# Optimization experiments

Measured on AMD Instinct MI355X. Metric: run time of the kernel, lower is better.

## Reference

```python
import jax, jax.numpy as jnp
import numpy as np
from math import sqrt

B, T, C = 2, 2048, 2048
H = 16
NOPE, ROPE, VD, LORA = 128, 64, 128, 512
QK = NOPE + ROPE  # 192
EPS = 1e-6


def _make_freq_cis(T, rope_dim):
    inv = 1.0 / (10000.0 ** (np.arange(0, rope_dim, 2, dtype=np.float32) / rope_dim))
    t = np.arange(T, dtype=np.float32)
    ang = np.outer(t, inv)  # [T, rope_dim/2]
    return jnp.asarray(np.stack([np.cos(ang), np.sin(ang)], -1))  # [T, rope_dim/2, 2]


def setup_inputs() -> dict:
    key = jax.random.key(0)
    ks = jax.random.split(key, 6)
    x = jax.random.normal(ks[0], (B, T, C), jnp.float32)
    freq_cis = _make_freq_cis(T, ROPE)
    causal = jnp.where(jnp.tril(jnp.ones((T, T), bool)), 0.0, -1e9).astype(jnp.float32)
    Wq = jax.random.normal(ks[1], (C, H * QK), jnp.float32) * (1.0 / sqrt(C))
    Wckv = jax.random.normal(ks[2], (C, LORA + ROPE), jnp.float32) * (1.0 / sqrt(C))
    kv_norm_w = jnp.ones((LORA,), jnp.float32)
    Wdkv = jax.random.normal(ks[3], (LORA, H * (NOPE + VD)), jnp.float32) * (1.0 / sqrt(LORA))
    Wproj = jax.random.normal(ks[4], (H * VD, C), jnp.float32) * (1.0 / sqrt(H * VD))
    return {"x": x, "freq_cis": freq_cis, "mask": causal, "window": causal,
            "Wq": Wq, "Wckv": Wckv, "kv_norm_w": kv_norm_w, "Wdkv": Wdkv,
            "Wproj": Wproj, "start_pos": 0}


def apply_rope(x, freq_cis):
    # x: [B, T, h, D]; freq_cis: [T, D/2, 2]
    b, t, h, d = x.shape
    xr = x.reshape(b, t, h, d // 2, 2)
    fc = freq_cis.reshape(1, t, 1, d // 2, 2)
    real = xr[..., 0] * fc[..., 0] - xr[..., 1] * fc[..., 1]
    imag = xr[..., 1] * fc[..., 0] + xr[..., 0] * fc[..., 1]
    return jnp.stack([real, imag], -1).reshape(b, t, h, d)


def rms_norm(x, w, eps=EPS):
    return x * jax.lax.rsqrt(jnp.mean(x * x, -1, keepdims=True) + eps) * w


def reference(x, freq_cis, mask, window, Wq, Wckv, kv_norm_w, Wdkv, Wproj, start_pos):
    del window, start_pos  # Global attention, no KV cache (prefill)
    b, t, _ = x.shape
    q = (x @ Wq).reshape(b, t, H, QK)
    q_nope, q_rope = q[..., :NOPE], q[..., NOPE:]
    q_rope = apply_rope(q_rope, freq_cis)

    ckv = x @ Wckv  # [B, T, LORA+ROPE]
    kv_lat, k_rope = ckv[..., :LORA], ckv[..., LORA:]
    k_rope = apply_rope(k_rope.reshape(b, t, 1, ROPE), freq_cis)  # [B,T,1,ROPE]

    kv = rms_norm(kv_lat, kv_norm_w) @ Wdkv  # [B, T, H*(NOPE+VD)]
    kv = kv.reshape(b, t, H, NOPE + VD)
    k_nope, v = kv[..., :NOPE], kv[..., NOPE:]

    q = jnp.concatenate([q_nope, q_rope], -1)                                   # [B,T,H,QK]
    k = jnp.concatenate([k_nope, jnp.broadcast_to(k_rope, (b, t, H, ROPE))], -1)

    scale = 1.0 / sqrt(QK)
    atten = jnp.einsum('bqhd,bkhd->bhqk', q, k) * scale + mask  # [B,H,T,T]
    atten = jax.nn.softmax(atten, -1)
    out = jnp.einsum('bhqk,bkhd->bqhd', atten, v).reshape(b, t, H * VD)
    return out @ Wproj
```

## Files before the change

kernel.cpp:

```cpp
#include <hip/hip_runtime.h>
#include <hip/hip_bf16.h>
#include <math.h>


typedef short bf16x8 __attribute__((ext_vector_type(8)));
typedef float f32x4 __attribute__((ext_vector_type(4)));
typedef float f32x16 __attribute__((ext_vector_type(16)));

#define MFMA16(a, b, c) __builtin_amdgcn_mfma_f32_16x16x32_bf16(a, b, c, 0, 0, 0)
#define MFMA32(a, b, c) __builtin_amdgcn_mfma_f32_32x32x16_bf16(a, b, c, 0, 0, 0)

__device__ __forceinline__ short f2bf(float f) {
  union { float f; unsigned u; } v; v.f = f;
  unsigned r = v.u + 0x7fffu + ((v.u >> 16) & 1u);
  return (short)(r >> 16);
}
__device__ __forceinline__ float bf2f(short s) {
  union { unsigned u; float f; } v;
  v.u = ((unsigned)(unsigned short)s) << 16;
  return v.f;
}
__device__ __forceinline__ unsigned cvtpk(float a, float b) {
  unsigned r;
  asm("v_cvt_pk_bf16_f32 %0, %1, %2" : "=v"(r) : "v"(a), "v"(b));
  return r;
}
__device__ __forceinline__ void gl16(const void* g, void* l) {
  __builtin_amdgcn_global_load_lds(
      (const __attribute__((address_space(1))) unsigned int*)g,
      (__attribute__((address_space(3))) unsigned int*)l, 16, 0, 0);
}
#define CFENCE() asm volatile("" ::: "memory")
#define HWBAR()  do { CFENCE(); __builtin_amdgcn_s_barrier(); CFENCE(); } while (0)

__global__ __launch_bounds__(256) void cvt_k(const float* __restrict__ in,
                                             short* __restrict__ out, int n) {
  int i = (blockIdx.x * 256 + threadIdx.x) * 8;
  if (i >= n) return;
  float4 a = *(const float4*)(in + i);
  float4 b = *(const float4*)(in + i + 4);
  bf16x8 o;
  o[0] = f2bf(a.x); o[1] = f2bf(a.y); o[2] = f2bf(a.z); o[3] = f2bf(a.w);
  o[4] = f2bf(b.x); o[5] = f2bf(b.y); o[6] = f2bf(b.z); o[7] = f2bf(b.w);
  *(bf16x8*)(out + i) = o;
}

__global__ __launch_bounds__(256) void tcvt_k(const float* __restrict__ W,
                                              short* __restrict__ out,
                                              int K, int N, int Np, int row_off) {
  __shared__ float tile[32][33];
  int k0 = blockIdx.x * 32, n0 = blockIdx.y * 32;
  int tx = threadIdx.x & 31, ty = threadIdx.x >> 5;
#pragma unroll
  for (int j = 0; j < 4; j++) {
    int k = k0 + ty + j * 8, n = n0 + tx;
    tile[ty + j * 8][tx] = (n < N) ? W[(size_t)k * N + n] : 0.f;
  }
  __syncthreads();
#pragma unroll
  for (int j = 0; j < 4; j++) {
    int n = n0 + ty + j * 8;
    out[(size_t)(row_off + n) * K + k0 + tx] = f2bf(tile[tx][ty + j * 8]);
  }
}

template <int MODE, int BM, int BN, int SGL>
__global__ __launch_bounds__(512, 2) void gemm8_k(const short* __restrict__ A,
                                                  const short* __restrict__ Bt,
                                                  void* __restrict__ C1,
                                                  void* __restrict__ C2,
                                                  int M, int N, int K, int nbx) {
  constexpr int FM = BM / 32;
  constexpr int FN = BN / 64;
  constexpr int XCH = (BM * 4) / 512;
  constexpr int YCH = (BN * 4) / 512;
  __shared__ short lX[3][BM * 32];
  __shared__ short lY[3][BN * 32];

  const int nwg = gridDim.x;
  const int cpx = nwg >> 3;
  const int swz = (blockIdx.x & 7) * cpx + (blockIdx.x >> 3);
  const int bx = swz % nbx, by = swz / nbx;
  const int m0 = bx * BM, n0 = by * BN;
  const int tid = threadIdx.x, lane = tid & 63, wave = tid >> 6;
  const int wm = wave >> 2, wn = wave & 3;
  const int l15 = lane & 15, l4 = lane >> 4;
  const int nt = K >> 5;

  auto stage = [&](int t) {
    int kk = t << 5;
    short* bX = &lX[t % 3][0];
    short* bY = &lY[t % 3][0];
#pragma unroll
    for (int c = 0; c < XCH; c++) {
      int idx = c * 512 + tid;
      int row = idx >> 2, seg = idx & 3;
      gl16(A + (size_t)(m0 + row) * K + kk + ((seg ^ ((row >> 1) & 3)) << 3),
           bX + idx * 8);
    }
#pragma unroll
    for (int c = 0; c < YCH; c++) {
      int idx = c * 512 + tid;
      int row = idx >> 2, seg = idx & 3;
      gl16(Bt + (size_t)(n0 + row) * K + kk + ((seg ^ ((row >> 1) & 3)) << 3),
           bY + idx * 8);
    }
  };

  f32x4 zero = {0.f, 0.f, 0.f, 0.f};
  f32x4 acc[FM][FN];
#pragma unroll
  for (int i = 0; i < FM; i++)
#pragma unroll
    for (int j = 0; j < FN; j++) acc[i][j] = zero;

  stage(0);
  stage(1);
  if constexpr (SGL == 4) asm volatile("s_waitcnt vmcnt(4)" ::: "memory");
  else                    asm volatile("s_waitcnt vmcnt(3)" ::: "memory");
  HWBAR();

  for (int t = 0; t < nt; t++) {
    const short* bX = &lX[t % 3][0];
    const short* bY = &lY[t % 3][0];
    bf16x8 xf[FM / 2], yf[FN];
#pragma unroll
    for (int i = 0; i < FM / 2; i++) {
      int row = wm * (BM / 2) + i * 16 + l15;
      xf[i] = *(const bf16x8*)&bX[row * 32 + ((l4 ^ ((row >> 1) & 3)) << 3)];
    }
#pragma unroll
    for (int j = 0; j < FN; j++) {
      int row = wn * (BN / 4) + j * 16 + l15;
      yf[j] = *(const bf16x8*)&bY[row * 32 + ((l4 ^ ((row >> 1) & 3)) << 3)];
    }
    bool st = (t + 2 < nt);
    if (st) stage(t + 2);
    HWBAR();
    __builtin_amdgcn_sched_barrier(0);
    __builtin_amdgcn_s_setprio(1);
#pragma unroll
    for (int i = 0; i < FM / 2; i++)
#pragma unroll
      for (int j = 0; j < FN; j++) acc[i][j] = MFMA16(xf[i], yf[j], acc[i][j]);
    __builtin_amdgcn_s_setprio(0);
    bf16x8 xg[FM / 2];
#pragma unroll
    for (int i = 0; i < FM / 2; i++) {
      int row = wm * (BM / 2) + (FM / 2 + i) * 16 + l15;
      xg[i] = *(const bf16x8*)&bX[row * 32 + ((l4 ^ ((row >> 1) & 3)) << 3)];
    }
    if (st) {
      if constexpr (SGL == 4) asm volatile("s_waitcnt vmcnt(4) lgkmcnt(0)" ::: "memory");
      else                    asm volatile("s_waitcnt vmcnt(3) lgkmcnt(0)" ::: "memory");
    } else {
      asm volatile("s_waitcnt vmcnt(0) lgkmcnt(0)" ::: "memory");
    }
    HWBAR();
    __builtin_amdgcn_sched_barrier(0);
    __builtin_amdgcn_s_setprio(1);
#pragma unroll
    for (int i = 0; i < FM / 2; i++)
#pragma unroll
      for (int j = 0; j < FN; j++)
        acc[FM / 2 + i][j] = MFMA16(xg[i], yf[j], acc[FM / 2 + i][j]);
    __builtin_amdgcn_s_setprio(0);
  }

#pragma unroll
  for (int i = 0; i < FM; i++) {
#pragma unroll
    for (int j = 0; j < FN; j++) {
#pragma unroll
      for (int r = 0; r < 4; r++) {
        int m = m0 + wm * (BM / 2) + i * 16 + l4 * 4 + r;
        int n = n0 + wn * (BN / 4) + j * 16 + l15;
        if (n >= N) continue;
        float v = acc[i][j][r];
        if (MODE == 0) {
          ((short*)C1)[(size_t)m * N + n] = f2bf(v);
        } else if (MODE == 1) {
          ((float*)C1)[(size_t)m * N + n] = v;
        } else {
          int bb = m >> 11, t2 = m & 2047, hh = n >> 8, c = n & 255;
          if (c < 128)
            ((short*)C1)[((size_t)(bb * 16 + hh) * 2048 + t2) * 192 + c] = f2bf(v);
          else
            ((short*)C2)[((size_t)(bb * 16 + hh) * 128 + (c - 128)) * 2048 + t2] = f2bf(v);
        }
      }
    }
  }
}

__global__ __launch_bounds__(256) void rmsnorm_k(const short* __restrict__ qc,
                                                 const float* __restrict__ w,
                                                 short* __restrict__ out) {
  int row = blockIdx.x * 4 + (threadIdx.x >> 6);
  int lane = threadIdx.x & 63;
  const short* src = qc + (size_t)row * 3712 + 3072 + lane * 8;
  bf16x8 v = *(const bf16x8*)src;
  float f[8];
  float ss = 0.f;
#pragma unroll
  for (int j = 0; j < 8; j++) { f[j] = bf2f(v[j]); ss += f[j] * f[j]; }
#pragma unroll
  for (int m = 1; m < 64; m <<= 1) ss += __shfl_xor(ss, m);
  float r = rsqrtf(ss * (1.f / 512.f) + 1e-6f);
  bf16x8 o;
#pragma unroll
  for (int j = 0; j < 8; j++) o[j] = f2bf(f[j] * r * w[lane * 8 + j]);
  *(bf16x8*)(out + (size_t)row * 512 + lane * 8) = o;
}

__global__ __launch_bounds__(256) void qrope_k(const short* __restrict__ qc,
                                               const float* __restrict__ freq,
                                               short* __restrict__ q_all) {
  int row = blockIdx.x * 4 + (threadIdx.x >> 6);
  int lane = threadIdx.x & 63;
  int b = row >> 15, h = (row >> 11) & 15, t = row & 2047;
  const short* src = qc + (size_t)(b * 2048 + t) * 3712 + h * 192;
  short* dst = q_all + (size_t)row * 192;
  const float scale = 0.10411756f;
  dst[lane] = f2bf(bf2f(src[lane]) * scale);
  dst[lane + 64] = f2bf(bf2f(src[lane + 64]) * scale);
  int p = lane >> 1;
  float c = freq[t * 64 + p * 2], s = freq[t * 64 + p * 2 + 1];
  float x0 = bf2f(src[128 + 2 * p]), x1 = bf2f(src[128 + 2 * p + 1]);
  float v = (lane & 1) ? (x1 * c + x0 * s) : (x0 * c - x1 * s);
  dst[128 + lane] = f2bf(v * scale);
}

__global__ __launch_bounds__(64) void krope_k(const short* __restrict__ qc,
                                              const float* __restrict__ freq,
                                              short* __restrict__ k_all) {
  int bt = blockIdx.x;
  int lane = threadIdx.x;
  int b = bt >> 11, t = bt & 2047;
  const short* src = qc + (size_t)bt * 3712 + 3584;
  int p = lane >> 1;
  float c = freq[t * 64 + p * 2], s = freq[t * 64 + p * 2 + 1];
  float x0 = bf2f(src[2 * p]), x1 = bf2f(src[2 * p + 1]);
  float v = (lane & 1) ? (x1 * c + x0 * s) : (x0 * c - x1 * s);
  short vb = f2bf(v);
#pragma unroll
  for (int h = 0; h < 16; h++)
    k_all[((size_t)(b * 16 + h) * 2048 + t) * 192 + 128 + lane] = vb;
}

__device__ __forceinline__ void stage6(const short* __restrict__ Kp,
                                       const short* __restrict__ VT,
                                       short* kb, short* vb, int kt, int ptid) {
#pragma unroll
  for (int c = 0; c < 6; c++) {
    int idx = c * 256 + ptid;
    if (idx < 832) {
      int r = idx / 25; if (r > 31) r = 31;
      int s = idx % 25;
      int s2 = (s >= 24) ? 0 : s;
      gl16(Kp + (size_t)(kt + r) * 192 + s2 * 8, kb + idx * 8);
    } else {
      int v = idx - 832;
      int r = v / 5; if (r > 127) r = 127;
      int s = v % 5;
      int s2 = (s >= 4) ? 0 : s;
      gl16(VT + (size_t)r * 2048 + kt + s2 * 8, vb + v * 8);
    }
  }
}

__global__ __launch_bounds__(512, 2) void attn_k(const short* __restrict__ q_all,
                                                 const short* __restrict__ k_all,
                                                 const short* __restrict__ vt,
                                                 short* __restrict__ attn_out) {
  __shared__ short kbuf[3][832 * 8];
  __shared__ short vbuf[3][704 * 8];
  int bh = blockIdx.x;
  int b = bh >> 4, h = bh & 15;
  int col = gridDim.y - 1 - blockIdx.y;
  int tid = threadIdx.x;
  int wave = tid >> 6, lane = tid & 63;
  int l31 = lane & 31, hi = lane >> 5;
  const bool producer = (wave >= 4);
  int qw = col * 128 + (wave & 3) * 32;
  int qrow = qw + l31;
  const short* Q = q_all + ((size_t)bh * 2048 + qrow) * 192;
  const short* Kp = k_all + (size_t)bh * 2048 * 192;
  const short* VT = vt + (size_t)bh * 128 * 2048;
  int sig = (l31 & 19) | ((l31 >> 1) & 4) | ((l31 << 1) & 8);

  bf16x8 qf[12];
  f32x16 o[4];
  f32x16 sInit, zro;
#pragma unroll
  for (int r = 0; r < 16; r++) { sInit[r] = -28.8539f; zro[r] = 0.f; }
  float lsum = 0.f;
  if (!producer) {
#pragma unroll
    for (int kb = 0; kb < 12; kb++)
      qf[kb] = *(const bf16x8*)(Q + kb * 16 + hi * 8);
#pragma unroll
    for (int vb = 0; vb < 4; vb++)
#pragma unroll
      for (int r = 0; r < 16; r++) o[vb][r] = 0.f;
  }

  const int nt = (col * 128 + 128) >> 5;

  if (producer) {
    stage6(Kp, VT, kbuf[0], vbuf[0], 0, tid - 256);
    if (nt > 1) stage6(Kp, VT, kbuf[1], vbuf[1], 32, tid - 256);
    asm volatile("s_waitcnt vmcnt(6)" ::: "memory");
  }
  HWBAR();

  for (int t = 0; t < nt; t++) {
    if (producer) {
      if (t + 2 < nt) {
        stage6(Kp, VT, kbuf[(t + 2) % 3], vbuf[(t + 2) % 3], (t + 2) << 5, tid - 256);
        asm volatile("s_waitcnt vmcnt(6)" ::: "memory");
      } else {
        asm volatile("s_waitcnt vmcnt(0)" ::: "memory");
      }
    } else {
      int kt = t << 5;
      int cur = t % 3;
      if (kt < qw + 32) {
        f32x16 sc = sInit, sc2 = zro;
        __builtin_amdgcn_s_setprio(1);
#pragma unroll
        for (int kb = 0; kb < 6; kb++) {
          int c0 = 2 * kb + hi, c1 = 2 * (kb + 6) + hi;
          bf16x8 kf0 = *(const bf16x8*)&kbuf[cur][sig * 200 + (c0 << 3)];
          bf16x8 kf1 = *(const bf16x8*)&kbuf[cur][sig * 200 + (c1 << 3)];
          sc = MFMA32(kf0, qf[kb], sc);
          sc2 = MFMA32(kf1, qf[kb + 6], sc2);
        }
        __builtin_amdgcn_s_setprio(0);
#pragma unroll
        for (int r = 0; r < 16; r++) sc[r] += sc2[r];
        unsigned pw[8];
        if (kt + 32 <= qw) {
#pragma unroll
          for (int r2 = 0; r2 < 8; r2++) {
            float pa = exp2f(sc[2 * r2]);
            float pb = exp2f(sc[2 * r2 + 1]);
            lsum += pa + pb;
            pw[r2] = cvtpk(pa, pb);
          }
        } else {
#pragma unroll
          for (int r2 = 0; r2 < 8; r2++) {
            int r = 2 * r2;
            int key = kt + (r & 3) + 4 * ((r >> 2) & 1) + 8 * hi + 16 * (r >> 3);
            float va = (key <= qrow) ? sc[r] : -1e30f;
            float vb2 = (key + 1 <= qrow) ? sc[r + 1] : -1e30f;
            float pa = exp2f(va);
            float pb = exp2f(vb2);
            lsum += pa + pb;
            pw[r2] = cvtpk(pa, pb);
          }
        }
        union { unsigned u[4]; bf16x8 v; } p0, p1;
#pragma unroll
        for (int w = 0; w < 4; w++) { p0.u[w] = pw[w]; p1.u[w] = pw[4 + w]; }
        __builtin_amdgcn_s_setprio(1);
#pragma unroll
        for (int vb = 0; vb < 4; vb++) {
          int vcol = vb * 32 + l31;
          bf16x8 vf0 = *(const bf16x8*)&vbuf[cur][vcol * 40 + (hi << 3)];
          bf16x8 vf1 = *(const bf16x8*)&vbuf[cur][vcol * 40 + ((2 + hi) << 3)];
          o[vb] = MFMA32(vf0, p0.v, o[vb]);
          o[vb] = MFMA32(vf1, p1.v, o[vb]);
        }
        __builtin_amdgcn_s_setprio(0);
      }
    }
    HWBAR();
  }

  if (!producer) {
    lsum += __shfl_xor(lsum, 32);
    float inv = 1.f / lsum;
    size_t base = ((size_t)b * 2048 + qrow) * 2048 + h * 128;
#pragma unroll
    for (int vb = 0; vb < 4; vb++) {
#pragma unroll
      for (int r2 = 0; r2 < 8; r2++) {
        int r = 2 * r2;
        int v = vb * 32 + (r & 3) + 8 * (r >> 2) + 4 * hi;
        unsigned pk2 = ((unsigned)(unsigned short)f2bf(o[vb][r] * inv)) |
                       (((unsigned)(unsigned short)f2bf(o[vb][r + 1] * inv)) << 16);
        *(unsigned*)(attn_out + base + v) = pk2;
      }
    }
  }
}

extern "C" void kernel_launch(void* const* d_in, const int* in_sizes, int n_in,
                              void* d_out, int out_size, void* d_ws, size_t ws_size,
                              hipStream_t stream) {
  const float* x = (const float*)d_in[0];
  const float* freq = (const float*)d_in[1];
  const float* Wq = (const float*)d_in[4];
  const float* Wckv = (const float*)d_in[5];
  const float* kvw = (const float*)d_in[6];
  const float* Wdkv = (const float*)d_in[7];
  const float* Wproj = (const float*)d_in[8];

  char* ws = (char*)d_ws;
  size_t off = 0;
  auto alloc = [&](size_t bytes) {
    size_t o = off;
    off += (bytes + 255) & ~(size_t)255;
    return o;
  };
  size_t o_xbf = alloc(4096ull * 2048 * 2);
  size_t o_wqc = alloc(3840ull * 2048 * 2);
  size_t o_wdkv = alloc(4096ull * 512 * 2);
  size_t o_wproj = alloc(2048ull * 2048 * 2);
  size_t o_qc = alloc(4096ull * 3712 * 2);
  size_t o_kvlat = alloc(4096ull * 512 * 2);
  size_t o_qall = alloc(32ull * 2048 * 192 * 2);
  size_t o_kall = alloc(32ull * 2048 * 192 * 2);
  size_t o_vt = alloc(32ull * 128 * 2048 * 2);
  size_t o_attn = o_xbf;

  short* x_bf = (short*)(ws + o_xbf);
  short* wqc = (short*)(ws + o_wqc);
  short* wdkv = (short*)(ws + o_wdkv);
  short* wproj = (short*)(ws + o_wproj);
  short* qc = (short*)(ws + o_qc);
  short* kvlat = (short*)(ws + o_kvlat);
  short* qall = (short*)(ws + o_qall);
  short* kall = (short*)(ws + o_kall);
  short* vtb = (short*)(ws + o_vt);
  short* attnb = (short*)(ws + o_attn);

  cvt_k<<<4096, 256, 0, stream>>>(x, x_bf, 4096 * 2048);
  tcvt_k<<<dim3(64, 96), 256, 0, stream>>>(Wq, wqc, 2048, 3072, 3072, 0);
  tcvt_k<<<dim3(64, 24), 256, 0, stream>>>(Wckv, wqc, 2048, 576, 768, 3072);
  tcvt_k<<<dim3(16, 128), 256, 0, stream>>>(Wdkv, wdkv, 512, 4096, 4096, 0);
  tcvt_k<<<dim3(64, 64), 256, 0, stream>>>(Wproj, wproj, 2048, 2048, 2048, 0);

  gemm8_k<0, 256, 256, 4><<<240, 512, 0, stream>>>(x_bf, wqc, qc, nullptr,
                                                   4096, 3712, 2048, 16);

  rmsnorm_k<<<1024, 256, 0, stream>>>(qc, kvw, kvlat);
  qrope_k<<<16384, 256, 0, stream>>>(qc, freq, qall);
  krope_k<<<4096, 64, 0, stream>>>(qc, freq, kall);

  gemm8_k<2, 256, 256, 4><<<256, 512, 0, stream>>>(kvlat, wdkv, kall, vtb,
                                                   4096, 4096, 512, 16);

  attn_k<<<dim3(32, 16), 512, 0, stream>>>(qall, kall, vtb, attnb);

  gemm8_k<1, 128, 256, 3><<<256, 512, 0, stream>>>(attnb, wproj, d_out, nullptr,
                                                   4096, 2048, 2048, 32);
}
```

Before: 287.1 us.

## Load V directly from global in attention, vectorize qrope and GEMM epilogue stores

The attention kernel stops staging V tiles through LDS with the producer waves. Consumer waves now load V fragments straight from global memory, issued early so they overlap the softmax math, and the freed LDS shrinks the buffers to K only. The qrope kernel is rewritten so each thread handles 8 contiguous bf16 values with vector loads and stores, and the launch size changes to match. The MODE-2 GEMM epilogue now packs the four transposed V values into one 8-byte store. The risk is that V global loads land on the critical path, since they are redundant across the four consumer waves and no longer prefetched.

New measurement: 315.2 us. +9.8%, slower.

```diff
diff --git a/kernel.cpp b/kernel.cpp
--- a/kernel.cpp
+++ b/kernel.cpp
@@ -4,6 +4,7 @@
 
 
 typedef short bf16x8 __attribute__((ext_vector_type(8)));
+typedef short short4v __attribute__((ext_vector_type(4)));
 typedef float f32x4 __attribute__((ext_vector_type(4)));
 typedef float f32x16 __attribute__((ext_vector_type(16)));
 
@@ -171,22 +172,30 @@
   for (int i = 0; i < FM; i++) {
 #pragma unroll
     for (int j = 0; j < FN; j++) {
-#pragma unroll
-      for (int r = 0; r < 4; r++) {
-        int m = m0 + wm * (BM / 2) + i * 16 + l4 * 4 + r;
-        int n = n0 + wn * (BN / 4) + j * 16 + l15;
-        if (n >= N) continue;
-        float v = acc[i][j][r];
-        if (MODE == 0) {
-          ((short*)C1)[(size_t)m * N + n] = f2bf(v);
-        } else if (MODE == 1) {
-          ((float*)C1)[(size_t)m * N + n] = v;
+      int m_ = m0 + wm * (BM / 2) + i * 16 + l4 * 4;
+      int n = n0 + wn * (BN / 4) + j * 16 + l15;
+      if (n >= N) continue;
+      if (MODE == 2) {
+        int bb = m_ >> 11, t2 = m_ & 2047, hh = n >> 8, c = n & 255;
+        if (c < 128) {
+#pragma unroll
+          for (int r = 0; r < 4; r++)
+            ((short*)C1)[((size_t)(bb * 16 + hh) * 2048 + t2 + r) * 192 + c] =
+                f2bf(acc[i][j][r]);
         } else {
-          int bb = m >> 11, t2 = m & 2047, hh = n >> 8, c = n & 255;
-          if (c < 128)
-            ((short*)C1)[((size_t)(bb * 16 + hh) * 2048 + t2) * 192 + c] = f2bf(v);
+          short4v pk;
+#pragma unroll
+          for (int r = 0; r < 4; r++) pk[r] = f2bf(acc[i][j][r]);
+          *(short4v*)&((short*)C2)[((size_t)(bb * 16 + hh) * 128 + (c - 128)) * 2048 + t2] = pk;
+        }
+      } else {
+#pragma unroll
+        for (int r = 0; r < 4; r++) {
+          float v = acc[i][j][r];
+          if (MODE == 0)
+            ((short*)C1)[(size_t)(m_ + r) * N + n] = f2bf(v);
           else
-            ((short*)C2)[((size_t)(bb * 16 + hh) * 128 + (c - 128)) * 2048 + t2] = f2bf(v);
+            ((float*)C1)[(size_t)(m_ + r) * N + n] = v;
         }
       }
     }
@@ -216,19 +225,34 @@
 __global__ __launch_bounds__(256) void qrope_k(const short* __restrict__ qc,
                                                const float* __restrict__ freq,
                                                short* __restrict__ q_all) {
-  int row = blockIdx.x * 4 + (threadIdx.x >> 6);
-  int lane = threadIdx.x & 63;
+  int g = blockIdx.x * 256 + threadIdx.x;
+  int row = g / 24, part = g % 24;
   int b = row >> 15, h = (row >> 11) & 15, t = row & 2047;
   const short* src = qc + (size_t)(b * 2048 + t) * 3712 + h * 192;
   short* dst = q_all + (size_t)row * 192;
   const float scale = 0.10411756f;
-  dst[lane] = f2bf(bf2f(src[lane]) * scale);
-  dst[lane + 64] = f2bf(bf2f(src[lane + 64]) * scale);
-  int p = lane >> 1;
-  float c = freq[t * 64 + p * 2], s = freq[t * 64 + p * 2 + 1];
-  float x0 = bf2f(src[128 + 2 * p]), x1 = bf2f(src[128 + 2 * p + 1]);
-  float v = (lane & 1) ? (x1 * c + x0 * s) : (x0 * c - x1 * s);
-  dst[128 + lane] = f2bf(v * scale);
+  if (part < 16) {
+    bf16x8 v = *(const bf16x8*)(src + part * 8);
+    bf16x8 o;
+#pragma unroll
+    for (int j = 0; j < 8; j++) o[j] = f2bf(bf2f(v[j]) * scale);
+    *(bf16x8*)(dst + part * 8) = o;
+  } else {
+    int q = part - 16;
+    bf16x8 v = *(const bf16x8*)(src + 128 + q * 8);
+    float4 fa = *(const float4*)(freq + t * 64 + q * 8);
+    float4 fb = *(const float4*)(freq + t * 64 + q * 8 + 4);
+    float cs[8] = {fa.x, fa.y, fa.z, fa.w, fb.x, fb.y, fb.z, fb.w};
+    bf16x8 o;
+#pragma unroll
+    for (int j = 0; j < 4; j++) {
+      float c = cs[2 * j], s = cs[2 * j + 1];
+      float x0 = bf2f(v[2 * j]), x1 = bf2f(v[2 * j + 1]);
+      o[2 * j] = f2bf((x0 * c - x1 * s) * scale);
+      o[2 * j + 1] = f2bf((x1 * c + x0 * s) * scale);
+    }
+    *(bf16x8*)(dst + 128 + q * 8) = o;
+  }
 }
 
 __global__ __launch_bounds__(64) void krope_k(const short* __restrict__ qc,
@@ -248,24 +272,15 @@
     k_all[((size_t)(b * 16 + h) * 2048 + t) * 192 + 128 + lane] = vb;
 }
 
-__device__ __forceinline__ void stage6(const short* __restrict__ Kp,
-                                       const short* __restrict__ VT,
-                                       short* kb, short* vb, int kt, int ptid) {
-#pragma unroll
-  for (int c = 0; c < 6; c++) {
+__device__ __forceinline__ void stageK(const short* __restrict__ Kp,
+                                       short* kb, int kt, int ptid) {
+#pragma unroll
+  for (int c = 0; c < 4; c++) {
     int idx = c * 256 + ptid;
-    if (idx < 832) {
-      int r = idx / 25; if (r > 31) r = 31;
-      int s = idx % 25;
-      int s2 = (s >= 24) ? 0 : s;
-      gl16(Kp + (size_t)(kt + r) * 192 + s2 * 8, kb + idx * 8);
-    } else {
-      int v = idx - 832;
-      int r = v / 5; if (r > 127) r = 127;
-      int s = v % 5;
-      int s2 = (s >= 4) ? 0 : s;
-      gl16(VT + (size_t)r * 2048 + kt + s2 * 8, vb + v * 8);
-    }
+    int r = idx / 25; if (r > 31) r = 31;
+    int s = idx % 25;
+    int s2 = (s >= 24) ? 0 : s;
+    gl16(Kp + (size_t)(kt + r) * 192 + s2 * 8, kb + idx * 8);
   }
 }
 
@@ -273,8 +288,7 @@
                                                  const short* __restrict__ k_all,
                                                  const short* __restrict__ vt,
                                                  short* __restrict__ attn_out) {
-  __shared__ short kbuf[3][832 * 8];
-  __shared__ short vbuf[3][704 * 8];
+  __shared__ short kbuf[3][1024 * 8];
   int bh = blockIdx.x;
   int b = bh >> 4, h = bh & 15;
   int col = gridDim.y - 1 - blockIdx.y;
@@ -308,17 +322,17 @@
   const int nt = (col * 128 + 128) >> 5;
 
   if (producer) {
-    stage6(Kp, VT, kbuf[0], vbuf[0], 0, tid - 256);
-    if (nt > 1) stage6(Kp, VT, kbuf[1], vbuf[1], 32, tid - 256);
-    asm volatile("s_waitcnt vmcnt(6)" ::: "memory");
+    stageK(Kp, kbuf[0], 0, tid - 256);
+    if (nt > 1) stageK(Kp, kbuf[1], 32, tid - 256);
+    asm volatile("s_waitcnt vmcnt(4)" ::: "memory");
   }
   HWBAR();
 
   for (int t = 0; t < nt; t++) {
     if (producer) {
       if (t + 2 < nt) {
-        stage6(Kp, VT, kbuf[(t + 2) % 3], vbuf[(t + 2) % 3], (t + 2) << 5, tid - 256);
-        asm volatile("s_waitcnt vmcnt(6)" ::: "memory");
+        stageK(Kp, kbuf[(t + 2) % 3], (t + 2) << 5, tid - 256);
+        asm volatile("s_waitcnt vmcnt(4)" ::: "memory");
       } else {
         asm volatile("s_waitcnt vmcnt(0)" ::: "memory");
       }
@@ -337,6 +351,10 @@
           sc2 = MFMA32(kf1, qf[kb + 6], sc2);
         }
         __builtin_amdgcn_s_setprio(0);
+        bf16x8 v00 = *(const bf16x8*)(VT + (size_t)l31 * 2048 + kt + (hi << 3));
+        bf16x8 v01 = *(const bf16x8*)(VT + (size_t)l31 * 2048 + kt + ((2 + hi) << 3));
+        bf16x8 v10 = *(const bf16x8*)(VT + (size_t)(32 + l31) * 2048 + kt + (hi << 3));
+        bf16x8 v11 = *(const bf16x8*)(VT + (size_t)(32 + l31) * 2048 + kt + ((2 + hi) << 3));
 #pragma unroll
         for (int r = 0; r < 16; r++) sc[r] += sc2[r];
         unsigned pw[8];
@@ -364,15 +382,15 @@
         union { unsigned u[4]; bf16x8 v; } p0, p1;
 #pragma unroll
         for (int w = 0; w < 4; w++) { p0.u[w] = pw[w]; p1.u[w] = pw[4 + w]; }
+        bf16x8 v20 = *(const bf16x8*)(VT + (size_t)(64 + l31) * 2048 + kt + (hi << 3));
+        bf16x8 v21 = *(const bf16x8*)(VT + (size_t)(64 + l31) * 2048 + kt + ((2 + hi) << 3));
+        bf16x8 v30 = *(const bf16x8*)(VT + (size_t)(96 + l31) * 2048 + kt + (hi << 3));
+        bf16x8 v31 = *(const bf16x8*)(VT + (size_t)(96 + l31) * 2048 + kt + ((2 + hi) << 3));
         __builtin_amdgcn_s_setprio(1);
-#pragma unroll
-        for (int vb = 0; vb < 4; vb++) {
-          int vcol = vb * 32 + l31;
-          bf16x8 vf0 = *(const bf16x8*)&vbuf[cur][vcol * 40 + (hi << 3)];
-          bf16x8 vf1 = *(const bf16x8*)&vbuf[cur][vcol * 40 + ((2 + hi) << 3)];
-          o[vb] = MFMA32(vf0, p0.v, o[vb]);
-          o[vb] = MFMA32(vf1, p1.v, o[vb]);
-        }
+        o[0] = MFMA32(v00, p0.v, o[0]); o[0] = MFMA32(v01, p1.v, o[0]);
+        o[1] = MFMA32(v10, p0.v, o[1]); o[1] = MFMA32(v11, p1.v, o[1]);
+        o[2] = MFMA32(v20, p0.v, o[2]); o[2] = MFMA32(v21, p1.v, o[2]);
+        o[3] = MFMA32(v30, p0.v, o[3]); o[3] = MFMA32(v31, p1.v, o[3]);
         __builtin_amdgcn_s_setprio(0);
       }
     }
@@ -447,7 +465,7 @@
                                                    4096, 3712, 2048, 16);
 
   rmsnorm_k<<<1024, 256, 0, stream>>>(qc, kvw, kvlat);
-  qrope_k<<<16384, 256, 0, stream>>>(qc, freq, qall);
+  qrope_k<<<6144, 256, 0, stream>>>(qc, freq, qall);
   krope_k<<<4096, 64, 0, stream>>>(qc, freq, kall);
 
   gemm8_k<2, 256, 256, 4><<<256, 512, 0, stream>>>(kvlat, wdkv, kall, vtb,
```
